# Optimization experiments

Hardware: AMD Instinct MI355X
Metric: run time of the kernel (lower is better)

## Reference

```python
import jax, jax.numpy as jnp
import numpy as np

B, N, C = 2, 2048, 1024
H = 16
D = C // H  # head_dim = 64

def setup_inputs() -> dict:
    key = jax.random.key(0)
    ks = jax.random.split(key, 5)
    s = 0.02
    return {
        "x": jax.random.normal(ks[0], (B, N, C), dtype=jnp.float32),
        "qkv_w": jax.random.normal(ks[1], (C, 3 * C), dtype=jnp.float32) * s,
        "qkv_b": jax.random.normal(ks[2], (3 * C,), dtype=jnp.float32) * s,
        "proj_w": jax.random.normal(ks[3], (C, C), dtype=jnp.float32) * s,
        "proj_b": jax.random.normal(ks[4], (C,), dtype=jnp.float32) * s,
    }

def reference(x, qkv_w, qkv_b, proj_w, proj_b):
    b, n, c = x.shape
    scale = (c // H) ** -0.5
    qkv = x @ qkv_w + qkv_b                      # (B, N, 3C)
    qkv = qkv.reshape(b, n, 3, H, D)
    q, k, v = jnp.moveaxis(qkv, 2, 0)            # each (B, N, H, D)
    # scores: (B, H, N, N)
    attn = jnp.einsum('bnhd,bmhd->bhnm', q, k) * scale
    attn = jax.nn.softmax(attn, axis=-1)
    out = jnp.einsum('bhnm,bmhd->bnhd', attn, v).reshape(b, n, c)
    out = out @ proj_w + proj_b
    return out
```

## Files before the change

### kernel.cpp

```cpp
#include <hip/hip_runtime.h>
#include <cstdint>
#include <cstddef>

typedef __bf16 bf16x8 __attribute__((ext_vector_type(8)));
typedef __bf16 bf16x2v __attribute__((ext_vector_type(2)));
typedef unsigned short u16;
typedef u16 u16x8v __attribute__((ext_vector_type(8)));
typedef float  f32x4  __attribute__((ext_vector_type(4)));
typedef unsigned int u32;

#define MFMA16(a, b, c) __builtin_amdgcn_mfma_f32_16x16x32_bf16((a), (b), (c), 0, 0, 0)
#define ASYNC16(g, l)                                                              \
  __builtin_amdgcn_global_load_lds(                                                \
      (const __attribute__((address_space(1))) unsigned int*)(g),                  \
      (__attribute__((address_space(3))) unsigned int*)(l), 16, 0, 0)

__device__ __forceinline__ u16 f2bf(float f) {
  unsigned u = __builtin_bit_cast(unsigned, f);
  u += 0x7fffu + ((u >> 16) & 1u);
  return (u16)(u >> 16);
}

__device__ __forceinline__ u32 cvt2(float a, float b) {
  bf16x2v t;
  t[0] = (__bf16)a;
  t[1] = (__bf16)b;
  return __builtin_bit_cast(u32, t);
}

#define SEQ 2048
#define CH  1024
#define NH  16
#define HD  64
#define QSCALE 0.18033688011112042f

__global__ void __launch_bounds__(256) cast_x_kernel(const float* __restrict__ in,
                                                     u16* __restrict__ out) {
  int i = blockIdx.x * 256 + threadIdx.x;
  float4 v = ((const float4*)in)[i];
  ushort4 o;
  o.x = f2bf(v.x); o.y = f2bf(v.y); o.z = f2bf(v.z); o.w = f2bf(v.w);
  ((ushort4*)out)[i] = o;
}

__global__ void __launch_bounds__(256) tcast_kernel(const float* __restrict__ in,
                                                    u16* __restrict__ out, int R, int C) {
  __shared__ u16 t[64][68];
  int c0 = blockIdx.x * 64, r0 = blockIdx.y * 64;
  int tx = threadIdx.x;
  int rr = tx >> 6, cc = tx & 63;
#pragma unroll
  for (int i = 0; i < 16; ++i) {
    int r = i * 4 + rr;
    t[r][cc] = f2bf(in[(size_t)(r0 + r) * C + c0 + cc]);
  }
  __syncthreads();
#pragma unroll
  for (int i = 0; i < 16; ++i) {
    int r = i * 4 + rr;
    out[(size_t)(c0 + r) * R + r0 + cc] = t[cc][r];
  }
}

__global__ void __launch_bounds__(256) tv_kernel(const u16* __restrict__ qkv,
                                                 u16* __restrict__ vt) {
  __shared__ u16 t[64][68];
  int n0 = blockIdx.x * 64;
  int bh = blockIdx.y;
  int b = bh >> 4, h = bh & 15;
  int tx = threadIdx.x;
  int rr = tx >> 6, cc = tx & 63;
  const u16* src = qkv + (size_t)(b * SEQ) * 3072 + 2048 + h * 64;
#pragma unroll
  for (int i = 0; i < 16; ++i) {
    int n = i * 4 + rr;
    t[n][cc] = src[(size_t)(n0 + n) * 3072 + cc];
  }
  __syncthreads();
  u16* dst = vt + (size_t)bh * 64 * SEQ;
#pragma unroll
  for (int i = 0; i < 16; ++i) {
    int d = i * 4 + rr;
    dst[(size_t)d * SEQ + n0 + cc] = t[cc][d];
  }
}

template <int MT>
__global__ void __launch_bounds__(256) gemm_kernel(const u16* __restrict__ A,
                                                   const u16* __restrict__ Bt,
                                                   const float* __restrict__ bias,
                                                   u16* __restrict__ outb,
                                                   float* __restrict__ outf,
                                                   int N, int K, int mode) {
  constexpr int R = MT * 32;
  __shared__ alignas(16) u16 As[R * 32];
  __shared__ alignas(16) u16 Bs[128 * 32];
  int tid = threadIdx.x;
  int lane = tid & 63, wave = tid >> 6;
  int wm = wave >> 1, wn = wave & 1;
  int qr = lane & 15, quad = lane >> 4;
  size_t rowA = (size_t)blockIdx.y * R;
  size_t rowB = (size_t)blockIdx.x * 128;
  int r0 = tid >> 2, c0 = (tid & 3) << 3;

  const u16* a0 = A + (rowA + r0) * K + c0;
  const u16* b0 = Bt + (rowB + r0) * K + c0;
  size_t step64 = (size_t)64 * K;
  u16* lA = &As[r0 * 32 + c0];
  u16* lB = &Bs[r0 * 32 + c0];

  f32x4 acc[MT][4];
#pragma unroll
  for (int mt = 0; mt < MT; ++mt)
#pragma unroll
    for (int nt = 0; nt < 4; ++nt) acc[mt][nt] = (f32x4){0.f, 0.f, 0.f, 0.f};

  for (int k0 = 0; k0 < K; k0 += 32) {
#pragma unroll
    for (int i = 0; i < R / 64; ++i)
      ASYNC16(a0 + k0 + i * step64, lA + i * 64 * 32);
    ASYNC16(b0 + k0, lB);
    ASYNC16(b0 + k0 + step64, lB + 64 * 32);
    __syncthreads();
    bf16x8 af[MT], bfr[4];
#pragma unroll
    for (int mt = 0; mt < MT; ++mt)
      af[mt] = *(const bf16x8*)&As[(wm * (MT * 16) + mt * 16 + qr) * 32 + quad * 8];
#pragma unroll
    for (int nt = 0; nt < 4; ++nt)
      bfr[nt] = *(const bf16x8*)&Bs[(wn * 64 + nt * 16 + qr) * 32 + quad * 8];
#pragma unroll
    for (int mt = 0; mt < MT; ++mt)
#pragma unroll
      for (int nt = 0; nt < 4; ++nt)
        acc[mt][nt] = MFMA16(af[mt], bfr[nt], acc[mt][nt]);
    __syncthreads();
  }

#pragma unroll
  for (int nt = 0; nt < 4; ++nt) {
    int col = (int)rowB + wn * 64 + nt * 16 + qr;
    float bv = bias[col];
#pragma unroll
    for (int mt = 0; mt < MT; ++mt) {
      size_t row = rowA + wm * (MT * 16) + mt * 16 + quad * 4;
#pragma unroll
      for (int r = 0; r < 4; ++r) {
        float v = acc[mt][nt][r] + bv;
        if (mode == 0) {
          if (col < 1024) v *= QSCALE;
          outb[(row + r) * N + col] = f2bf(v);
        } else {
          outf[(row + r) * N + col] = v;
        }
      }
    }
  }
}

__global__ void __launch_bounds__(256) attn_kernel(const u16* __restrict__ qkv,
                                                   const u16* __restrict__ vt,
                                                   u16* __restrict__ out) {
  __shared__ alignas(16) u16 kbuf[2][64 * 64];
  __shared__ alignas(16) u16 vbuf[2][64 * 64];
  __shared__ alignas(16) u16 pbuf[4][32 * 64];
  int bh = blockIdx.x;
  int b = bh >> 4, h = bh & 15;
  int m0 = blockIdx.y * 128;
  int tid = threadIdx.x;
  int lane = tid & 63, wave = tid >> 6;
  int qr = lane & 15, quad = lane >> 4;

  const u16* kbase = qkv + (size_t)(b * SEQ) * 3072 + 1024 + h * 64;
  const u16* vtbase = vt + (size_t)bh * 64 * SEQ;
  u16* pw = &pbuf[wave][0];

  int srow0 = wave * 16 + (lane >> 3);
  int scs0 = (lane & 7) ^ (srow0 & 7);
  int srow1 = srow0 + 8;
  int scs1 = (lane & 7) ^ (srow1 & 7);

  const u16* qbase = qkv + (size_t)(b * SEQ + m0 + wave * 32) * 3072 + h * 64;
  bf16x8 qf[2][2];
#pragma unroll
  for (int mt = 0; mt < 2; ++mt)
#pragma unroll
    for (int ks = 0; ks < 2; ++ks)
      qf[mt][ks] = *(const bf16x8*)&qbase[(size_t)(mt * 16 + qr) * 3072 + ks * 32 + quad * 8];

  const bf16x8 vone = __builtin_bit_cast(bf16x8, (u16x8v)((u16)0x3F80));

  f32x4 o[2][4], l5[2];
#pragma unroll
  for (int mt = 0; mt < 2; ++mt) {
    l5[mt] = (f32x4){0.f, 0.f, 0.f, 0.f};
#pragma unroll
    for (int dt = 0; dt < 4; ++dt) o[mt][dt] = (f32x4){0.f, 0.f, 0.f, 0.f};
  }

  ASYNC16(kbase + (size_t)srow0 * 3072 + scs0 * 8, &kbuf[0][wave * 1024 + lane * 8]);
  ASYNC16(kbase + (size_t)srow1 * 3072 + scs1 * 8, &kbuf[0][wave * 1024 + 512 + lane * 8]);
  ASYNC16(vtbase + (size_t)srow0 * 2048 + scs0 * 8, &vbuf[0][wave * 1024 + lane * 8]);
  ASYNC16(vtbase + (size_t)srow1 * 2048 + scs1 * 8, &vbuf[0][wave * 1024 + 512 + lane * 8]);

  for (int t = 0; t < 32; ++t) {
    int cur = t & 1;
    __syncthreads();

    if (t + 1 < 32) {
      int nx = (t + 1) * 64;
      int o2 = cur ^ 1;
      ASYNC16(kbase + (size_t)(nx + srow0) * 3072 + scs0 * 8, &kbuf[o2][wave * 1024 + lane * 8]);
      ASYNC16(kbase + (size_t)(nx + srow1) * 3072 + scs1 * 8, &kbuf[o2][wave * 1024 + 512 + lane * 8]);
      ASYNC16(vtbase + (size_t)srow0 * 2048 + nx + scs0 * 8, &vbuf[o2][wave * 1024 + lane * 8]);
      ASYNC16(vtbase + (size_t)srow1 * 2048 + nx + scs1 * 8, &vbuf[o2][wave * 1024 + 512 + lane * 8]);
    }

    const u16* kb = &kbuf[cur][0];
    const u16* vb = &vbuf[cur][0];

    bf16x8 kf[4][2];
#pragma unroll
    for (int nt = 0; nt < 4; ++nt)
#pragma unroll
      for (int ks = 0; ks < 2; ++ks)
        kf[nt][ks] = *(const bf16x8*)&kb[(nt * 16 + qr) * 64 + (((ks * 4 + quad) ^ (qr & 7)) << 3)];

#pragma unroll
    for (int mt = 0; mt < 2; ++mt)
#pragma unroll
      for (int nt = 0; nt < 4; ++nt) {
        f32x4 z = (f32x4){0.f, 0.f, 0.f, 0.f};
        z = MFMA16(kf[nt][0], qf[mt][0], z);
        z = MFMA16(kf[nt][1], qf[mt][1], z);
        float p0 = __builtin_amdgcn_exp2f(z[0]);
        float p1 = __builtin_amdgcn_exp2f(z[1]);
        float p2 = __builtin_amdgcn_exp2f(z[2]);
        float p3 = __builtin_amdgcn_exp2f(z[3]);
        uint2 pk;
        pk.x = cvt2(p0, p1);
        pk.y = cvt2(p2, p3);
        int nb = nt * 16 + quad * 4;
        int addr = (mt * 16 + qr) * 64 + ((((nb >> 3) ^ (qr & 7)) << 3) | (nb & 7));
        *(uint2*)&pw[addr] = pk;
      }

    bf16x8 vf[4][2];
#pragma unroll
    for (int dt = 0; dt < 4; ++dt)
#pragma unroll
      for (int ks = 0; ks < 2; ++ks)
        vf[dt][ks] = *(const bf16x8*)&vb[(dt * 16 + qr) * 64 + (((ks * 4 + quad) ^ (qr & 7)) << 3)];

    bf16x8 pf[2][2];
#pragma unroll
    for (int mt = 0; mt < 2; ++mt)
#pragma unroll
      for (int ks = 0; ks < 2; ++ks)
        pf[mt][ks] =
            *(const bf16x8*)&pw[(mt * 16 + qr) * 64 + (((ks * 4 + quad) ^ (qr & 7)) << 3)];

#pragma unroll
    for (int mt = 0; mt < 2; ++mt) {
#pragma unroll
      for (int dt = 0; dt < 4; ++dt) {
        o[mt][dt] = MFMA16(pf[mt][0], vf[dt][0], o[mt][dt]);
        o[mt][dt] = MFMA16(pf[mt][1], vf[dt][1], o[mt][dt]);
      }
      l5[mt] = MFMA16(pf[mt][0], vone, l5[mt]);
      l5[mt] = MFMA16(pf[mt][1], vone, l5[mt]);
    }
  }

  u16* obase = out + (size_t)(b * SEQ + m0 + wave * 32) * CH + h * 64;
#pragma unroll
  for (int mt = 0; mt < 2; ++mt)
#pragma unroll
    for (int r = 0; r < 4; ++r) {
      float inv = 1.0f / l5[mt][r];
#pragma unroll
      for (int dt = 0; dt < 4; ++dt)
        obase[(size_t)(mt * 16 + quad * 4 + r) * CH + dt * 16 + qr] = f2bf(o[mt][dt][r] * inv);
    }
}

extern "C" void kernel_launch(void* const* d_in, const int* in_sizes, int n_in,
                              void* d_out, int out_size, void* d_ws, size_t ws_size,
                              hipStream_t stream) {
  const float* x      = (const float*)d_in[0];
  const float* qkv_w  = (const float*)d_in[1];
  const float* qkv_b  = (const float*)d_in[2];
  const float* proj_w = (const float*)d_in[3];
  const float* proj_b = (const float*)d_in[4];
  float* out = (float*)d_out;

  char* w = (char*)d_ws;
  u16* qkv_bf = (u16*)w;
  u16* xb     = (u16*)(w + 25165824);
  u16* wprojt = (u16*)(w + 25165824 + 8388608);
  u16* wqkvt  = (u16*)(w + 25165824 + 8388608 + 2097152);
  u16* attn_bf = xb;
  u16* vt      = wqkvt;

  cast_x_kernel<<<4096, 256, 0, stream>>>(x, xb);
  tcast_kernel<<<dim3(48, 16), 256, 0, stream>>>(qkv_w, wqkvt, 1024, 3072);
  tcast_kernel<<<dim3(16, 16), 256, 0, stream>>>(proj_w, wprojt, 1024, 1024);
  gemm_kernel<4><<<dim3(24, 32), 256, 0, stream>>>(xb, wqkvt, qkv_b, qkv_bf, nullptr, 3072, 1024, 0);
  tv_kernel<<<dim3(32, 32), 256, 0, stream>>>(qkv_bf, vt);
  attn_kernel<<<dim3(32, 16), 256, 0, stream>>>(qkv_bf, vt, attn_bf);
  gemm_kernel<2><<<dim3(8, 64), 256, 0, stream>>>(attn_bf, wprojt, proj_b, nullptr, out, 1024, 1024, 1);
}
```

Before: 213.1 us.

## Merge prep casts into one launch and stage 128-key tiles in attention

Folds the x cast and the two weight transpose-casts into a single prep kernel that dispatches on block index, so two kernel launches go away. The attention kernel now stages K/V tiles of 128 keys per iteration and processes them as two 64-key sub-steps, which halves the number of block barriers and async-copy rounds. The cost is double the LDS for the K/V buffers, which may lower occupancy.

```diff
diff --git a/kernel.cpp b/kernel.cpp
--- a/kernel.cpp
+++ b/kernel.cpp
@@ -34,20 +34,33 @@
 #define HD  64
 #define QSCALE 0.18033688011112042f
 
-__global__ void __launch_bounds__(256) cast_x_kernel(const float* __restrict__ in,
-                                                     u16* __restrict__ out) {
-  int i = blockIdx.x * 256 + threadIdx.x;
-  float4 v = ((const float4*)in)[i];
-  ushort4 o;
-  o.x = f2bf(v.x); o.y = f2bf(v.y); o.z = f2bf(v.z); o.w = f2bf(v.w);
-  ((ushort4*)out)[i] = o;
-}
-
-__global__ void __launch_bounds__(256) tcast_kernel(const float* __restrict__ in,
-                                                    u16* __restrict__ out, int R, int C) {
+__global__ void __launch_bounds__(256) prep_kernel(const float* __restrict__ x,
+                                                   const float* __restrict__ qkv_w,
+                                                   const float* __restrict__ proj_w,
+                                                   u16* __restrict__ xb,
+                                                   u16* __restrict__ wqkvt,
+                                                   u16* __restrict__ wprojt) {
   __shared__ u16 t[64][68];
-  int c0 = blockIdx.x * 64, r0 = blockIdx.y * 64;
+  int bx = blockIdx.x;
   int tx = threadIdx.x;
+  if (bx < 4096) {
+    int i = bx * 256 + tx;
+    float4 v = ((const float4*)x)[i];
+    ushort4 o;
+    o.x = f2bf(v.x); o.y = f2bf(v.y); o.z = f2bf(v.z); o.w = f2bf(v.w);
+    ((ushort4*)xb)[i] = o;
+    return;
+  }
+  const float* in; u16* out; int R, C, c0, r0;
+  if (bx < 4096 + 768) {
+    int i = bx - 4096;
+    in = qkv_w; out = wqkvt; R = 1024; C = 3072;
+    c0 = (i % 48) * 64; r0 = (i / 48) * 64;
+  } else {
+    int i = bx - 4864;
+    in = proj_w; out = wprojt; R = 1024; C = 1024;
+    c0 = (i % 16) * 64; r0 = (i / 16) * 64;
+  }
   int rr = tx >> 6, cc = tx & 63;
 #pragma unroll
   for (int i = 0; i < 16; ++i) {
@@ -161,8 +174,8 @@
 __global__ void __launch_bounds__(256) attn_kernel(const u16* __restrict__ qkv,
                                                    const u16* __restrict__ vt,
                                                    u16* __restrict__ out) {
-  __shared__ alignas(16) u16 kbuf[2][64 * 64];
-  __shared__ alignas(16) u16 vbuf[2][64 * 64];
+  __shared__ alignas(16) u16 kbuf[2][128 * 64];
+  __shared__ alignas(16) u16 vbuf[2][64 * 128];
   __shared__ alignas(16) u16 pbuf[4][32 * 64];
   int bh = blockIdx.x;
   int b = bh >> 4, h = bh & 15;
@@ -175,10 +188,8 @@
   const u16* vtbase = vt + (size_t)bh * 64 * SEQ;
   u16* pw = &pbuf[wave][0];
 
-  int srow0 = wave * 16 + (lane >> 3);
-  int scs0 = (lane & 7) ^ (srow0 & 7);
-  int srow1 = srow0 + 8;
-  int scs1 = (lane & 7) ^ (srow1 & 7);
+  int klr = lane >> 3;
+  int kcs = (lane & 7) ^ klr;
 
   const u16* qbase = qkv + (size_t)(b * SEQ + m0 + wave * 32) * 3072 + h * 64;
   bf16x8 qf[2][2];
@@ -198,77 +209,88 @@
     for (int dt = 0; dt < 4; ++dt) o[mt][dt] = (f32x4){0.f, 0.f, 0.f, 0.f};
   }
 
-  ASYNC16(kbase + (size_t)srow0 * 3072 + scs0 * 8, &kbuf[0][wave * 1024 + lane * 8]);
-  ASYNC16(kbase + (size_t)srow1 * 3072 + scs1 * 8, &kbuf[0][wave * 1024 + 512 + lane * 8]);
-  ASYNC16(vtbase + (size_t)srow0 * 2048 + scs0 * 8, &vbuf[0][wave * 1024 + lane * 8]);
-  ASYNC16(vtbase + (size_t)srow1 * 2048 + scs1 * 8, &vbuf[0][wave * 1024 + 512 + lane * 8]);
-
-  for (int t = 0; t < 32; ++t) {
+  auto stage = [&](int buf, int n0) {
+#pragma unroll
+    for (int i = 0; i < 4; ++i) {
+      int kr = wave * 32 + i * 8 + klr;
+      ASYNC16(kbase + (size_t)(n0 + kr) * 3072 + kcs * 8,
+              &kbuf[buf][(wave * 32 + i * 8) * 64 + lane * 8]);
+    }
+#pragma unroll
+    for (int i = 0; i < 4; ++i) {
+      int vr = wave * 16 + i * 4 + (lane >> 4);
+      int vcs = ((lane & 7) ^ (vr & 7)) | (lane & 8);
+      ASYNC16(vtbase + (size_t)vr * 2048 + n0 + vcs * 8,
+              &vbuf[buf][(wave * 16 + i * 4) * 128 + lane * 8]);
+    }
+  };
+
+  stage(0, 0);
+
+  for (int t = 0; t < 16; ++t) {
     int cur = t & 1;
     __syncthreads();
 
-    if (t + 1 < 32) {
-      int nx = (t + 1) * 64;
-      int o2 = cur ^ 1;
-      ASYNC16(kbase + (size_t)(nx + srow0) * 3072 + scs0 * 8, &kbuf[o2][wave * 1024 + lane * 8]);
-      ASYNC16(kbase + (size_t)(nx + srow1) * 3072 + scs1 * 8, &kbuf[o2][wave * 1024 + 512 + lane * 8]);
-      ASYNC16(vtbase + (size_t)srow0 * 2048 + nx + scs0 * 8, &vbuf[o2][wave * 1024 + lane * 8]);
-      ASYNC16(vtbase + (size_t)srow1 * 2048 + nx + scs1 * 8, &vbuf[o2][wave * 1024 + 512 + lane * 8]);
-    }
-
-    const u16* kb = &kbuf[cur][0];
-    const u16* vb = &vbuf[cur][0];
-
-    bf16x8 kf[4][2];
-#pragma unroll
-    for (int nt = 0; nt < 4; ++nt)
-#pragma unroll
-      for (int ks = 0; ks < 2; ++ks)
-        kf[nt][ks] = *(const bf16x8*)&kb[(nt * 16 + qr) * 64 + (((ks * 4 + quad) ^ (qr & 7)) << 3)];
-
-#pragma unroll
-    for (int mt = 0; mt < 2; ++mt)
-#pragma unroll
-      for (int nt = 0; nt < 4; ++nt) {
-        f32x4 z = (f32x4){0.f, 0.f, 0.f, 0.f};
-        z = MFMA16(kf[nt][0], qf[mt][0], z);
-        z = MFMA16(kf[nt][1], qf[mt][1], z);
-        float p0 = __builtin_amdgcn_exp2f(z[0]);
-        float p1 = __builtin_amdgcn_exp2f(z[1]);
-        float p2 = __builtin_amdgcn_exp2f(z[2]);
-        float p3 = __builtin_amdgcn_exp2f(z[3]);
-        uint2 pk;
-        pk.x = cvt2(p0, p1);
-        pk.y = cvt2(p2, p3);
-        int nb = nt * 16 + quad * 4;
-        int addr = (mt * 16 + qr) * 64 + ((((nb >> 3) ^ (qr & 7)) << 3) | (nb & 7));
-        *(uint2*)&pw[addr] = pk;
+    if (t + 1 < 16) stage(cur ^ 1, (t + 1) * 128);
+
+#pragma unroll
+    for (int sp = 0; sp < 2; ++sp) {
+      const u16* kb = &kbuf[cur][sp * 64 * 64];
+      const u16* vb = &vbuf[cur][0];
+
+      bf16x8 kf[4][2];
+#pragma unroll
+      for (int nt = 0; nt < 4; ++nt)
+#pragma unroll
+        for (int ks = 0; ks < 2; ++ks)
+          kf[nt][ks] =
+              *(const bf16x8*)&kb[(nt * 16 + qr) * 64 + (((ks * 4 + quad) ^ (qr & 7)) << 3)];
+
+#pragma unroll
+      for (int mt = 0; mt < 2; ++mt)
+#pragma unroll
+        for (int nt = 0; nt < 4; ++nt) {
+          f32x4 z = (f32x4){0.f, 0.f, 0.f, 0.f};
+          z = MFMA16(kf[nt][0], qf[mt][0], z);
+          z = MFMA16(kf[nt][1], qf[mt][1], z);
+          float p0 = __builtin_amdgcn_exp2f(z[0]);
+          float p1 = __builtin_amdgcn_exp2f(z[1]);
+          float p2 = __builtin_amdgcn_exp2f(z[2]);
+          float p3 = __builtin_amdgcn_exp2f(z[3]);
+          uint2 pk;
+          pk.x = cvt2(p0, p1);
+          pk.y = cvt2(p2, p3);
+          int nb = nt * 16 + quad * 4;
+          int addr = (mt * 16 + qr) * 64 + ((((nb >> 3) ^ (qr & 7)) << 3) | (nb & 7));
+          *(uint2*)&pw[addr] = pk;
+        }
+
+      bf16x8 vf[4][2];
+#pragma unroll
+      for (int dt = 0; dt < 4; ++dt)
+#pragma unroll
+        for (int ks = 0; ks < 2; ++ks)
+          vf[dt][ks] = *(const bf16x8*)&vb[(dt * 16 + qr) * 128 +
+                                           ((sp * 8 + ((ks * 4 + quad) ^ (qr & 7))) << 3)];
+
+      bf16x8 pf[2][2];
+#pragma unroll
+      for (int mt = 0; mt < 2; ++mt)
+#pragma unroll
+        for (int ks = 0; ks < 2; ++ks)
+          pf[mt][ks] =
+              *(const bf16x8*)&pw[(mt * 16 + qr) * 64 + (((ks * 4 + quad) ^ (qr & 7)) << 3)];
+
+#pragma unroll
+      for (int mt = 0; mt < 2; ++mt) {
+#pragma unroll
+        for (int dt = 0; dt < 4; ++dt) {
+          o[mt][dt] = MFMA16(pf[mt][0], vf[dt][0], o[mt][dt]);
+          o[mt][dt] = MFMA16(pf[mt][1], vf[dt][1], o[mt][dt]);
+        }
+        l5[mt] = MFMA16(pf[mt][0], vone, l5[mt]);
+        l5[mt] = MFMA16(pf[mt][1], vone, l5[mt]);
       }
-
-    bf16x8 vf[4][2];
-#pragma unroll
-    for (int dt = 0; dt < 4; ++dt)
-#pragma unroll
-      for (int ks = 0; ks < 2; ++ks)
-        vf[dt][ks] = *(const bf16x8*)&vb[(dt * 16 + qr) * 64 + (((ks * 4 + quad) ^ (qr & 7)) << 3)];
-
-    bf16x8 pf[2][2];
-#pragma unroll
-    for (int mt = 0; mt < 2; ++mt)
-#pragma unroll
-      for (int ks = 0; ks < 2; ++ks)
-        pf[mt][ks] =
-            *(const bf16x8*)&pw[(mt * 16 + qr) * 64 + (((ks * 4 + quad) ^ (qr & 7)) << 3)];
-
-#pragma unroll
-    for (int mt = 0; mt < 2; ++mt) {
-#pragma unroll
-      for (int dt = 0; dt < 4; ++dt) {
-        o[mt][dt] = MFMA16(pf[mt][0], vf[dt][0], o[mt][dt]);
-        o[mt][dt] = MFMA16(pf[mt][1], vf[dt][1], o[mt][dt]);
-      }
-      l5[mt] = MFMA16(pf[mt][0], vone, l5[mt]);
-      l5[mt] = MFMA16(pf[mt][1], vone, l5[mt]);
     }
   }
 
@@ -302,9 +324,7 @@
   u16* attn_bf = xb;
   u16* vt      = wqkvt;
 
-  cast_x_kernel<<<4096, 256, 0, stream>>>(x, xb);
-  tcast_kernel<<<dim3(48, 16), 256, 0, stream>>>(qkv_w, wqkvt, 1024, 3072);
-  tcast_kernel<<<dim3(16, 16), 256, 0, stream>>>(proj_w, wprojt, 1024, 1024);
+  prep_kernel<<<5120, 256, 0, stream>>>(x, qkv_w, proj_w, xb, wqkvt, wprojt);
   gemm_kernel<4><<<dim3(24, 32), 256, 0, stream>>>(xb, wqkvt, qkv_b, qkv_bf, nullptr, 3072, 1024, 0);
   tv_kernel<<<dim3(32, 32), 256, 0, stream>>>(qkv_bf, vt);
   attn_kernel<<<dim3(32, 16), 256, 0, stream>>>(qkv_bf, vt, attn_bf);
```

Result: faster. 204.9 us (-3.8%).
